# Optimization experiments

Measured on AMD Instinct MI355X. Metric: run time of the kernel, lower is better.

The kernel has to match this reference:

```python
import jax, jax.numpy as jnp
import numpy as np
import math

D_MODEL = 1024
NHEAD = 16
FACTOR = 1
B, L = 2, 4096


def setup_inputs() -> dict:
    key = jax.random.key(0)
    ks = jax.random.split(key, 12)
    s = 0.02
    inp = {
        "query": jax.random.normal(ks[0], (B, L, D_MODEL), dtype=jnp.float32),
        "key": jax.random.normal(ks[1], (B, L, D_MODEL), dtype=jnp.float32),
        "value": jax.random.normal(ks[2], (B, L, D_MODEL), dtype=jnp.float32),
        "Wq": jax.random.normal(ks[3], (D_MODEL, D_MODEL), dtype=jnp.float32) * s,
        "bq": jnp.zeros((D_MODEL,), dtype=jnp.float32),
        "Wk": jax.random.normal(ks[4], (D_MODEL, D_MODEL), dtype=jnp.float32) * s,
        "bk": jnp.zeros((D_MODEL,), dtype=jnp.float32),
        "Wv": jax.random.normal(ks[5], (D_MODEL, D_MODEL), dtype=jnp.float32) * s,
        "bv": jnp.zeros((D_MODEL,), dtype=jnp.float32),
        "Wo": jax.random.normal(ks[6], (D_MODEL, D_MODEL), dtype=jnp.float32) * s,
        "bo": jnp.zeros((D_MODEL,), dtype=jnp.float32),
    }
    return inp


def _autocorr_forward(query, key, value, Wq, bq, Wk, bk, Wv, bv, Wo, bo):
    Bq, Lq, d = query.shape
    Lk = key.shape[1]
    H = NHEAD
    Dk = d // H

    # projections, split heads -> (B, H, L, Dk)
    Q = (query @ Wq + bq).reshape(Bq, Lq, H, Dk).transpose(0, 2, 1, 3)
    K = (key @ Wk + bk).reshape(Bq, Lk, H, Dk).transpose(0, 2, 1, 3)
    V = (value @ Wv + bv).reshape(Bq, Lk, H, Dk).transpose(0, 2, 1, 3)

    # align K/V sequence length to L_q (truncate or zero-pad)
    if Lk > Lq:
        K = K[:, :, :Lq, :]
        V = V[:, :, :Lq, :]
    elif Lq > Lk:
        pad = [(0, 0), (0, 0), (0, Lq - Lk), (0, 0)]
        K = jnp.pad(K, pad)
        V = jnp.pad(V, pad)
    Lloc = Lq

    # FFT-based circular autocorrelation along the sequence axis
    Qf = jnp.fft.rfft(Q, axis=2)
    Kf = jnp.fft.rfft(K, axis=2)
    corr = jnp.fft.irfft(Qf * jnp.conj(Kf), n=Lloc, axis=2)  # (B,H,L,Dk)
    corr_mean = corr.mean(axis=-1)  # (B,H,L)

    top_k = min(max(1, int(FACTOR * math.log(Lloc + 1))), Lloc)
    w, idx = jax.lax.top_k(corr_mean, top_k)  # (B,H,k)
    w = jax.nn.softmax(w, axis=-1)

    # circular gather of V at each delay, weighted combine over top-k delays
    ar = jnp.arange(Lloc)
    shifted = (ar[None, None, None, :] + idx[..., None]) % Lloc  # (B,H,k,L)
    rolled = jnp.take_along_axis(
        V[:, :, None, :, :], shifted[..., None], axis=3
    )  # (B,H,k,L,Dk)
    out = jnp.einsum("bhk,bhkld->bhld", w, rolled)  # (B,H,L,Dk)

    out = out.transpose(0, 2, 1, 3).reshape(Bq, Lq, d)
    return out @ Wo + bo  # dropout is identity in eval mode


def reference(query, key, value, Wq, bq, Wk, bk, Wv, bv, Wo, bo):
    return _autocorr_forward(query, key, value, Wq, bq, Wk, bk, Wv, bv, Wo, bo)
```

## Files before the change

### kernel.cpp

```cpp
#include <hip/hip_runtime.h>
#include <hip/hip_bf16.h>

#define LL 4096
#define NH 16
#define DM 1024
#define DK 64
#define MTOT 8192
#define PI_F 3.14159265358979323846f

typedef short short8 __attribute__((ext_vector_type(8)));
typedef float f32x4 __attribute__((ext_vector_type(4)));

typedef __attribute__((address_space(1))) const unsigned char g_u8;
typedef __attribute__((address_space(3))) unsigned char l_u8;

__device__ __forceinline__ void gload16(const void* g, void* l){
  __builtin_amdgcn_global_load_lds((g_u8*)g, (l_u8*)l, 16, 0, 0);
}

__device__ __forceinline__ unsigned short f2bf(float x){
  union { float f; unsigned int u; } v; v.f = x;
  unsigned int r = v.u + 0x7FFFu + ((v.u >> 16) & 1u);
  return (unsigned short)(r >> 16);
}
__device__ __forceinline__ float bf2f(unsigned short u){
  union { unsigned int u; float f; } v; v.u = ((unsigned int)u) << 16; return v.f;
}

__global__ void k_conv_x(const float* __restrict__ in, unsigned short* __restrict__ out, int n4){
  int i = blockIdx.x*256 + threadIdx.x;
  if (i >= n4) return;
  float4 v = ((const float4*)in)[i];
  ushort4 o; o.x=f2bf(v.x); o.y=f2bf(v.y); o.z=f2bf(v.z); o.w=f2bf(v.w);
  ((ushort4*)out)[i] = o;
}

__global__ void k_conv_x_split2(const float* __restrict__ q, const float* __restrict__ k,
                                unsigned short* __restrict__ hi, unsigned short* __restrict__ lo, int n4){
  int i = blockIdx.x*256 + threadIdx.x;
  float4 v = (i < n4) ? ((const float4*)q)[i] : ((const float4*)k)[i - n4];
  ushort4 oh, ol;
  oh.x=f2bf(v.x); ol.x=f2bf(v.x - bf2f(oh.x));
  oh.y=f2bf(v.y); ol.y=f2bf(v.y - bf2f(oh.y));
  oh.z=f2bf(v.z); ol.z=f2bf(v.z - bf2f(oh.z));
  oh.w=f2bf(v.w); ol.w=f2bf(v.w - bf2f(oh.w));
  ((ushort4*)hi)[i] = oh;
  ((ushort4*)lo)[i] = ol;
}

__global__ void k_conv_wt(const float* __restrict__ W0, const float* __restrict__ W1,
                          const float* __restrict__ W2, const float* __restrict__ W3,
                          unsigned short* __restrict__ hi_base, unsigned short* __restrict__ lo_base){
  const float* W = (blockIdx.z==0)?W0:(blockIdx.z==1)?W1:(blockIdx.z==2)?W2:W3;
  unsigned short* oh = hi_base + (size_t)blockIdx.z*DM*DM;
  unsigned short* ol = (blockIdx.z<2) ? (lo_base + (size_t)blockIdx.z*DM*DM) : nullptr;
  __shared__ unsigned short th[64][65];
  __shared__ unsigned short tl[64][65];
  int n0 = blockIdx.x*64, k0 = blockIdx.y*64;
  for (int i=0;i<16;i++){
    int g = i*256 + threadIdx.x;
    int kr = g>>6, nc = g&63;
    float x = W[(size_t)(k0+kr)*DM + n0+nc];
    unsigned short h = f2bf(x);
    th[kr][nc] = h;
    tl[kr][nc] = f2bf(x - bf2f(h));
  }
  __syncthreads();
  for (int i=0;i<16;i++){
    int g = i*256 + threadIdx.x;
    int nr = g>>6, kc = g&63;
    oh[(size_t)(n0+nr)*DM + k0+kc] = th[kc][nr];
    if (ol) ol[(size_t)(n0+nr)*DM + k0+kc] = tl[kc][nr];
  }
}

template<int MODE>
__global__ __launch_bounds__(256) void k_gemm_plain(
    const short* __restrict__ A, const short* __restrict__ Bt,
    const float* __restrict__ bias, float* __restrict__ Cf, unsigned short* __restrict__ Cb)
{
  __shared__ short As[128][64];
  __shared__ short Bs[128][64];
  const int m0 = blockIdx.x*128, n0 = blockIdx.y*128;
  const int tid = threadIdx.x;
  const int wave = tid>>6, lane = tid&63;
  const int wm = (wave>>1)*64, wn = (wave&1)*64;
  const int li = lane&15, lk4 = lane>>4;
  const int srow = lane>>3;
  const int scol = (((lane&7) ^ srow))*8;
  f32x4 acc[4][4] = {};
  for (int kt=0; kt<16; ++kt){
    #pragma unroll
    for (int c=0;c<4;c++){
      int q = wave*4+c;
      int row = q*8 + srow;
      gload16(&A [(size_t)(m0+row)*DM + kt*64 + scol], &As[q*8][0]);
      gload16(&Bt[(size_t)(n0+row)*DM + kt*64 + scol], &Bs[q*8][0]);
    }
    __syncthreads();
    #pragma unroll
    for (int kk=0; kk<64; kk+=32){
      short8 af[4], bfv[4];
      #pragma unroll
      for (int mi=0;mi<4;mi++)
        af[mi] = *(const short8*)&As[wm+mi*16+li][((( (kk>>3)+lk4 ) ^ (li&7)))*8];
      #pragma unroll
      for (int ni=0;ni<4;ni++)
        bfv[ni] = *(const short8*)&Bs[wn+ni*16+li][((( (kk>>3)+lk4 ) ^ (li&7)))*8];
      #pragma unroll
      for (int mi=0;mi<4;mi++)
        #pragma unroll
        for (int ni=0;ni<4;ni++)
          acc[mi][ni] = __builtin_amdgcn_mfma_f32_16x16x32_bf16(af[mi], bfv[ni], acc[mi][ni], 0,0,0);
    }
    __syncthreads();
  }
  #pragma unroll
  for (int mi=0;mi<4;mi++){
    #pragma unroll
    for (int ni=0;ni<4;ni++){
      const int col = n0 + wn + ni*16 + li;
      const float bv = bias[col];
      const int mbase = m0 + wm + mi*16 + lk4*4;
      #pragma unroll
      for (int r=0;r<4;r++){
        const int row = mbase + r;
        float v = acc[mi][ni][r] + bv;
        if (MODE==2){
          Cf[(size_t)row*DM + col] = v;
        } else {
          int b = row>>12, l = row&(LL-1), h = col>>6, d = col&63;
          Cb[(((size_t)(b*NH+h))*LL + l)*DK + d] = f2bf(v);
        }
      }
    }
  }
}

__global__ __launch_bounds__(512, 2) void k_gemm_split256(
    const short* __restrict__ Ahi, const short* __restrict__ Alo,
    const short* __restrict__ Whi, const short* __restrict__ Wlo,
    const float* __restrict__ bias_q, const float* __restrict__ bias_k,
    float* __restrict__ OutQ, float* __restrict__ OutK, int nq)
{
  __shared__ short AsH[2][256][32];
  __shared__ short AsL[2][256][32];
  __shared__ short BsH[2][256][32];
  __shared__ short BsL[2][256][32];

  const int side = (blockIdx.x >= nq) ? 1 : 0;
  const int m0 = blockIdx.x*256, n0 = blockIdx.y*256;
  const short* Bhi = Whi + (size_t)side*DM*DM;
  const short* Blo = Wlo + (size_t)side*DM*DM;
  const float* bias = side ? bias_k : bias_q;
  float* Ct = side ? OutK : OutQ;
  const int ml0 = m0 - side*(nq*256);

  const int tid = threadIdx.x;
  const int wave = tid>>6, lane = tid&63;
  const int wm = (wave>>2)*128;
  const int wn = (wave&3)*64;
  const int li = lane&15, lk4 = lane>>4;

  const int sr = lane>>2, sc4 = lane&3;
  const int scol = ((sc4 ^ (sr&3) ^ ((sr>>2)&3)))*8;
  const int rbyte = ((lk4 ^ (li&3) ^ (li>>2)))*8;

  f32x4 acc[8][4] = {};

  auto STAGE_HALF = [&](int kt, int bufi, int h){
    const int r0 = h*128 + wave*16;
    const int gr = r0 + sr;
    const int kof = kt*32 + scol;
    gload16(&Ahi[(size_t)(m0+gr)*DM + kof], &AsH[bufi][r0][0]);
    gload16(&Alo[(size_t)(m0+gr)*DM + kof], &AsL[bufi][r0][0]);
    gload16(&Bhi[(size_t)(n0+gr)*DM + kof], &BsH[bufi][r0][0]);
    gload16(&Blo[(size_t)(n0+gr)*DM + kof], &BsL[bufi][r0][0]);
  };

  STAGE_HALF(0, 0, 0);
  STAGE_HALF(0, 0, 1);

  for (int kt=0; kt<32; ++kt){
    const int cur = kt&1;
    if (kt < 31){
      STAGE_HALF(kt+1, cur^1, 0);
      asm volatile("s_waitcnt vmcnt(4)" ::: "memory");
    } else {
      asm volatile("s_waitcnt vmcnt(0)" ::: "memory");
    }
    asm volatile("" ::: "memory");
    __builtin_amdgcn_s_barrier();
    asm volatile("" ::: "memory");

    short8 bhf[4], blf[4];
    #pragma unroll
    for (int ni=0;ni<4;ni++){
      bhf[ni] = *(const short8*)&BsH[cur][wn+ni*16+li][rbyte];
      blf[ni] = *(const short8*)&BsL[cur][wn+ni*16+li][rbyte];
    }
    #pragma unroll
    for (int p=0;p<4;p++){
      if (p==2 && kt<31) STAGE_HALF(kt+1, cur^1, 1);
      short8 ah0 = *(const short8*)&AsH[cur][wm+(2*p  )*16+li][rbyte];
      short8 al0 = *(const short8*)&AsL[cur][wm+(2*p  )*16+li][rbyte];
      short8 ah1 = *(const short8*)&AsH[cur][wm+(2*p+1)*16+li][rbyte];
      short8 al1 = *(const short8*)&AsL[cur][wm+(2*p+1)*16+li][rbyte];
      __builtin_amdgcn_s_setprio(1);
      #pragma unroll
      for (int ni=0;ni<4;ni++){
        f32x4 a0 = acc[2*p][ni];
        a0 = __builtin_amdgcn_mfma_f32_16x16x32_bf16(ah0, bhf[ni], a0, 0,0,0);
        a0 = __builtin_amdgcn_mfma_f32_16x16x32_bf16(ah0, blf[ni], a0, 0,0,0);
        a0 = __builtin_amdgcn_mfma_f32_16x16x32_bf16(al0, bhf[ni], a0, 0,0,0);
        acc[2*p][ni] = a0;
        f32x4 a1 = acc[2*p+1][ni];
        a1 = __builtin_amdgcn_mfma_f32_16x16x32_bf16(ah1, bhf[ni], a1, 0,0,0);
        a1 = __builtin_amdgcn_mfma_f32_16x16x32_bf16(ah1, blf[ni], a1, 0,0,0);
        a1 = __builtin_amdgcn_mfma_f32_16x16x32_bf16(al1, bhf[ni], a1, 0,0,0);
        acc[2*p+1][ni] = a1;
      }
      __builtin_amdgcn_s_setprio(0);
    }
    asm volatile("" ::: "memory");
    __builtin_amdgcn_s_barrier();
    asm volatile("" ::: "memory");
  }

  #pragma unroll
  for (int mi=0;mi<8;mi++){
    #pragma unroll
    for (int ni=0;ni<4;ni++){
      const int col = n0 + wn + ni*16 + li;
      const float bv = bias[col];
      const int mbase = ml0 + wm + mi*16 + lk4*4;
      const int b = mbase>>12, l0 = mbase&(LL-1);
      const int h = col>>6, d = col&63;
      float4 o;
      o.x = acc[mi][ni][0]+bv; o.y = acc[mi][ni][1]+bv;
      o.z = acc[mi][ni][2]+bv; o.w = acc[mi][ni][3]+bv;
      *(float4*)&Ct[(((size_t)(b*NH+h))*DK + d)*LL + l0] = o;
    }
  }
}

__device__ __forceinline__ float2 cmul(float2 a, float2 b){
  return make_float2(a.x*b.x - a.y*b.y, a.x*b.y + a.y*b.x);
}
__device__ __forceinline__ int swz(int i){ return i ^ ((i>>4)&15); }

__device__ __forceinline__ float2 ctw(float2 v, int k, float sgn){
  float c, s;
  switch(k){
    case 0: return v;
    case 1: c= 0.92387953251f; s= 0.38268343236f; break;
    case 2: c= 0.70710678119f; s= 0.70710678119f; break;
    case 3: c= 0.38268343236f; s= 0.92387953251f; break;
    case 4: c= 0.f;            s= 1.f;            break;
    case 6: c=-0.70710678119f; s= 0.70710678119f; break;
    default:c=-0.92387953251f; s=-0.38268343236f; break;
  }
  s *= sgn;
  return make_float2(v.x*c - v.y*s, v.x*s + v.y*c);
}

template<int SGN>
__device__ __forceinline__ void dft16(float2 x[16]){
  const float sg = (float)SGN;
  #pragma unroll
  for (int m1=0;m1<4;m1++){
    float2 a=x[m1], b=x[m1+4], c=x[m1+8], d=x[m1+12];
    float acx=a.x+c.x, acy=a.y+c.y, sx=a.x-c.x, sy=a.y-c.y;
    float bdx=b.x+d.x, bdy=b.y+d.y, tx=b.x-d.x, ty=b.y-d.y;
    float ix=-sg*ty, iy=sg*tx;
    x[m1]    = make_float2(acx+bdx, acy+bdy);
    x[m1+4]  = make_float2(sx+ix,  sy+iy);
    x[m1+8]  = make_float2(acx-bdx, acy-bdy);
    x[m1+12] = make_float2(sx-ix,  sy-iy);
  }
  float2 y[16];
  #pragma unroll
  for (int p1=0;p1<4;p1++){
    float2 a = x[4*p1+0];
    float2 b = ctw(x[4*p1+1], p1,   sg);
    float2 c = ctw(x[4*p1+2], 2*p1, sg);
    float2 d = ctw(x[4*p1+3], 3*p1, sg);
    float acx=a.x+c.x, acy=a.y+c.y, sx=a.x-c.x, sy=a.y-c.y;
    float bdx=b.x+d.x, bdy=b.y+d.y, tx=b.x-d.x, ty=b.y-d.y;
    float ix=-sg*ty, iy=sg*tx;
    y[p1]    = make_float2(acx+bdx, acy+bdy);
    y[p1+4]  = make_float2(sx+ix,  sy+iy);
    y[p1+8]  = make_float2(acx-bdx, acy-bdy);
    y[p1+12] = make_float2(sx-ix,  sy-iy);
  }
  #pragma unroll
  for (int i=0;i<16;i++) x[i]=y[i];
}

template<int SGN>
__device__ __forceinline__ void twiddle_apply(float2 x[16], int j, float invden){
  float th = (float)SGN * 6.28318530717958647f * (float)j * invden;
  float s, c; __sincosf(th, &s, &c);
  float2 w1 = make_float2(c, s);
  float2 w2 = cmul(w1,w1), w3 = cmul(w2,w1), w4 = cmul(w2,w2);
  float2 w8 = cmul(w4,w4), w12 = cmul(w8,w4);
  float2 wl[4] = {make_float2(1.f,0.f), w1, w2, w3};
  float2 wh[4] = {make_float2(1.f,0.f), w4, w8, w12};
  #pragma unroll
  for (int m=1;m<16;m++){
    float2 tw = cmul(wh[m>>2], wl[m&3]);
    x[m] = cmul(x[m], tw);
  }
}

template<int SGN>
__device__ __forceinline__ void fft_stages(float2* lds, float2 x[16], int t){
  dft16<SGN>(x);
  #pragma unroll
  for (int p=0;p<16;p++) lds[swz(t*16+p)] = x[p];
  __syncthreads();
  #pragma unroll
  for (int m=0;m<16;m++) x[m] = lds[swz(t + 256*m)];
  __syncthreads();
  twiddle_apply<SGN>(x, t&15, 1.0f/256.0f);
  dft16<SGN>(x);
  {
    int base = (t>>4)*256 + (t&15);
    #pragma unroll
    for (int p=0;p<16;p++) lds[swz(base + 16*p)] = x[p];
  }
  __syncthreads();
  #pragma unroll
  for (int m=0;m<16;m++) x[m] = lds[swz(t + 256*m)];
  __syncthreads();
  twiddle_apply<SGN>(x, t, 1.0f/4096.0f);
  dft16<SGN>(x);
  #pragma unroll
  for (int p=0;p<16;p++) lds[swz(t + 256*p)] = x[p];
  __syncthreads();
}

__global__ __launch_bounds__(256) void k_fft_fwd(const float* __restrict__ Qt, const float* __restrict__ Kt,
                                                 float* __restrict__ Spart){
  __shared__ float2 lds[4096];
  const int bh = blockIdx.x >> 4, g = blockIdx.x & 15;
  const int t = threadIdx.x;
  float2 pacc[16];
  #pragma unroll
  for (int i=0;i<16;i++) pacc[i]=make_float2(0.f,0.f);
  for (int dd=0; dd<4; ++dd){
    const size_t base = ((size_t)bh*DK + g*4 + dd)*LL;
    float2 x[16];
    #pragma unroll
    for (int m=0;m<16;m++){
      int n = t + 256*m;
      x[m] = make_float2(Qt[base+n], Kt[base+n]);
    }
    fft_stages<-1>(lds, x, t);
    #pragma unroll
    for (int i=0;i<16;i++){
      int f = t + 256*i;
      float2 A = lds[swz(f)];
      float2 Bv = lds[swz((LL-f)&(LL-1))];
      float qr = 0.5f*(A.x+Bv.x), qi = 0.5f*(A.y-Bv.y);
      float kr = 0.5f*(A.y+Bv.y), ki = -0.5f*(A.x-Bv.x);
      pacc[i].x += qr*kr + qi*ki;
      pacc[i].y += qi*kr - qr*ki;
    }
    __syncthreads();
  }
  float2* Sp = (float2*)Spart + (size_t)blockIdx.x*LL;
  #pragma unroll
  for (int i=0;i<16;i++) Sp[t + 256*i] = pacc[i];
}

__global__ __launch_bounds__(256) void k_ifft_topk(const float* __restrict__ Spart,
                                                   float* __restrict__ w8, int* __restrict__ idx8){
  __shared__ float2 lds[4096];
  __shared__ float c[4096];
  __shared__ float rv[256];
  __shared__ int   ri[256];
  __shared__ float topv[8];
  __shared__ int   topi[8];
  const int bh = blockIdx.x, t = threadIdx.x;
  float2 x[16];
  #pragma unroll
  for (int m=0;m<16;m++){
    float2 acc = make_float2(0.f,0.f);
    int n = t + 256*m;
    for (int g2=0; g2<16; ++g2){
      float2 v = ((const float2*)Spart)[((size_t)bh*16+g2)*LL + n];
      acc.x += v.x; acc.y += v.y;
    }
    x[m] = acc;
  }
  fft_stages<1>(lds, x, t);
  const float scale = 1.0f/((float)LL * (float)DK);
  #pragma unroll
  for (int m=0;m<16;m++){ int f=t+256*m; c[f] = lds[swz(f)].x * scale; }
  __syncthreads();
  for (int kk=0; kk<8; kk++){
    float bv = -3.4e38f; int bi = 0;
    #pragma unroll
    for (int i=0;i<16;i++){
      int f = t + 256*i;
      float v = c[f];
      if (v > bv || (v == bv && f < bi)) { bv = v; bi = f; }
    }
    rv[t]=bv; ri[t]=bi;
    __syncthreads();
    for (int off=128; off>0; off>>=1){
      if (t < off){
        float ov = rv[t+off]; int oi = ri[t+off];
        if (ov > rv[t] || (ov == rv[t] && oi < ri[t])) { rv[t]=ov; ri[t]=oi; }
      }
      __syncthreads();
    }
    if (t==0){ topv[kk]=rv[0]; topi[kk]=ri[0]; c[ri[0]] = -3.0e38f; }
    __syncthreads();
  }
  if (t==0){
    float m = topv[0];
    float e[8], sum=0.f;
    for (int k=0;k<8;k++){ e[k]=__expf(topv[k]-m); sum+=e[k]; }
    for (int k=0;k<8;k++){ w8[bh*8+k]=e[k]/sum; idx8[bh*8+k]=topi[k]; }
  }
}

__global__ __launch_bounds__(256) void k_gather(const unsigned short* __restrict__ Vh,
                                                const float* __restrict__ w8, const int* __restrict__ idx8,
                                                unsigned short* __restrict__ Ob){
  const int blk = blockIdx.x;
  const int bh = blk >> 6;
  const int l0 = (blk & 63) * 64;
  const int b = bh >> 4, h = bh & 15;
  float w[8]; int ix[8];
  #pragma unroll
  for (int k=0;k<8;k++){ w[k]=w8[bh*8+k]; ix[k]=idx8[bh*8+k]; }
  const int tid = threadIdx.x;
  for (int it=0; it<16; ++it){
    int e = it*256 + tid;
    int lo = e >> 6, d = e & 63;
    int l = l0 + lo;
    float acc = 0.f;
    #pragma unroll
    for (int k=0;k<8;k++){
      int sl = (l + ix[k]) & (LL-1);
      acc += w[k] * bf2f(Vh[((size_t)bh*LL + sl)*DK + d]);
    }
    Ob[((size_t)(b*LL + l))*DM + h*DK + d] = f2bf(acc);
  }
}

extern "C" void kernel_launch(void* const* d_in, const int* in_sizes, int n_in,
                              void* d_out, int out_size, void* d_ws, size_t ws_size,
                              hipStream_t stream) {
  const float* query = (const float*)d_in[0];
  const float* key   = (const float*)d_in[1];
  const float* value = (const float*)d_in[2];
  const float* Wq = (const float*)d_in[3];
  const float* bq = (const float*)d_in[4];
  const float* Wk = (const float*)d_in[5];
  const float* bk = (const float*)d_in[6];
  const float* Wv = (const float*)d_in[7];
  const float* bv = (const float*)d_in[8];
  const float* Wo = (const float*)d_in[9];
  const float* bo = (const float*)d_in[10];
  float* out = (float*)d_out;

  char* ws = (char*)d_ws;
  const int n4 = MTOT*DM/4;
  const size_t MB16 = (size_t)MTOT*DM*2;

  size_t off = 0;
  auto take = [&](size_t b)->char*{ char* p = ws + off; off += (b + 255) & ~(size_t)255; return p; };

  const size_t merged_bytes = 2*(2*MB16) + (size_t)4*DM*DM*2 + (size_t)2*DM*DM*2
                            + 2*((size_t)2*NH*DK*LL*4) + 16384;

  if (ws_size >= merged_bytes) {
    short* Xs_hi = (short*)take(2*MB16);
    short* Xs_lo = (short*)take(2*MB16);
    short* Wth = (short*)take((size_t)4*DM*DM*2);
    short* Wtl = (short*)take((size_t)2*DM*DM*2);
    float* Qt  = (float*)take((size_t)2*NH*DK*LL*4);
    float* Kt  = (float*)take((size_t)2*NH*DK*LL*4);
    float* w8  = (float*)take(32*8*4);
    int*  idx8 = (int*)take(32*8*4);
    float* Spart = (float*)Xs_hi;
    unsigned short* Ob = (unsigned short*)((char*)Xs_hi + MB16);
    unsigned short* Xv = (unsigned short*)Xs_lo;
    unsigned short* Vh = (unsigned short*)((char*)Xs_lo + MB16);

    k_conv_wt<<<dim3(16,16,4),256,0,stream>>>(Wq,Wk,Wv,Wo,(unsigned short*)Wth,(unsigned short*)Wtl);
    k_conv_x_split2<<<2*n4/256,256,0,stream>>>(query,key,(unsigned short*)Xs_hi,(unsigned short*)Xs_lo,n4);
    k_gemm_split256<<<dim3(64,4),512,0,stream>>>(Xs_hi, Xs_lo, Wth, Wtl, bq, bk, Qt, Kt, 32);
    k_conv_x<<<n4/256,256,0,stream>>>(value, Xv, n4);
    k_gemm_plain<1><<<dim3(64,8),256,0,stream>>>((const short*)Xv, Wth + (size_t)2*DM*DM, bv, nullptr, Vh);
    k_fft_fwd<<<512,256,0,stream>>>(Qt, Kt, Spart);
    k_ifft_topk<<<32,256,0,stream>>>(Spart, w8, idx8);
    k_gather<<<2048,256,0,stream>>>(Vh, w8, idx8, Ob);
    k_gemm_plain<2><<<dim3(64,8),256,0,stream>>>((const short*)Ob, Wth + (size_t)3*DM*DM, bo, out, nullptr);
  } else {
    short* Xhi = (short*)take(MB16);
    short* Xlo = (short*)take(MB16);
    short* Wth = (short*)take((size_t)4*DM*DM*2);
    short* Wtl = (short*)take((size_t)2*DM*DM*2);
    float* Qt  = (float*)take((size_t)2*NH*DK*LL*4);
    float* Kt  = (float*)take((size_t)2*NH*DK*LL*4);
    unsigned short* Vh = (unsigned short*)take((size_t)2*NH*LL*DK*2);
    float* w8  = (float*)take(32*8*4);
    int*  idx8 = (int*)take(32*8*4);
    float* Spart = (float*)Xlo;

    k_conv_wt<<<dim3(16,16,4),256,0,stream>>>(Wq,Wk,Wv,Wo,(unsigned short*)Wth,(unsigned short*)Wtl);

    k_conv_x_split2<<<n4/256,256,0,stream>>>(query,query,(unsigned short*)Xhi,(unsigned short*)Xlo,n4);
    k_gemm_split256<<<dim3(32,4),512,0,stream>>>(Xhi, Xlo, Wth, Wtl, bq, bq, Qt, Qt, 32);

    k_conv_x_split2<<<n4/256,256,0,stream>>>(key,key,(unsigned short*)Xhi,(unsigned short*)Xlo,n4);
    k_gemm_split256<<<dim3(32,4),512,0,stream>>>(Xhi, Xlo, Wth + (size_t)DM*DM, Wtl + (size_t)DM*DM,
                                                 bk, bk, Kt, Kt, 32);

    k_conv_x<<<n4/256,256,0,stream>>>(value,(unsigned short*)Xhi,n4);
    k_gemm_plain<1><<<dim3(64,8),256,0,stream>>>(Xhi, Wth + (size_t)2*DM*DM, bv, nullptr, Vh);

    k_fft_fwd<<<512,256,0,stream>>>(Qt, Kt, Spart);
    k_ifft_topk<<<32,256,0,stream>>>(Spart, w8, idx8);
    k_gather<<<2048,256,0,stream>>>(Vh, w8, idx8, (unsigned short*)Xhi);

    k_gemm_plain<2><<<dim3(64,8),256,0,stream>>>(Xhi, Wth + (size_t)3*DM*DM, bo, out, nullptr);
  }
}
```

Measured before the change: 250.8 us.

## Fuse V projection GEMM into merged Q/K split-precision GEMM launch

Extends the merged Q/K split-bf16 GEMM kernel with a third block range that computes the V projection in single bf16 and writes head-major bf16 output. A new workspace tier lays out separate buffers so the V input conversion and all three projections run in one 96x4 grid, removing the separate k_gemm_plain<1> launch. The intent is to cut launch overhead and fill the GPU better with more blocks. The risk is that V blocks use a 256-tile, 512-thread config with scalar strided stores, and the extra register and LDS pressure from the new branch could affect the Q/K path.

```diff
diff --git a/kernel.cpp b/kernel.cpp
--- a/kernel.cpp
+++ b/kernel.cpp
@@ -139,22 +139,22 @@
 
 __global__ __launch_bounds__(512, 2) void k_gemm_split256(
     const short* __restrict__ Ahi, const short* __restrict__ Alo,
+    const short* __restrict__ Av,
     const short* __restrict__ Whi, const short* __restrict__ Wlo,
+    const short* __restrict__ Wvh,
     const float* __restrict__ bias_q, const float* __restrict__ bias_k,
-    float* __restrict__ OutQ, float* __restrict__ OutK, int nq)
+    const float* __restrict__ bias_v,
+    float* __restrict__ OutQ, float* __restrict__ OutK,
+    unsigned short* __restrict__ OutV, int nq)
 {
   __shared__ short AsH[2][256][32];
   __shared__ short AsL[2][256][32];
   __shared__ short BsH[2][256][32];
   __shared__ short BsL[2][256][32];
 
-  const int side = (blockIdx.x >= nq) ? 1 : 0;
-  const int m0 = blockIdx.x*256, n0 = blockIdx.y*256;
-  const short* Bhi = Whi + (size_t)side*DM*DM;
-  const short* Blo = Wlo + (size_t)side*DM*DM;
-  const float* bias = side ? bias_k : bias_q;
-  float* Ct = side ? OutK : OutQ;
-  const int ml0 = m0 - side*(nq*256);
+  const int bx = blockIdx.x;
+  const int side = (bx >= 2*nq) ? 2 : (bx >= nq) ? 1 : 0;
+  const int n0 = blockIdx.y*256;
 
   const int tid = threadIdx.x;
   const int wave = tid>>6, lane = tid&63;
@@ -168,78 +168,152 @@
 
   f32x4 acc[8][4] = {};
 
-  auto STAGE_HALF = [&](int kt, int bufi, int h){
-    const int r0 = h*128 + wave*16;
-    const int gr = r0 + sr;
-    const int kof = kt*32 + scol;
-    gload16(&Ahi[(size_t)(m0+gr)*DM + kof], &AsH[bufi][r0][0]);
-    gload16(&Alo[(size_t)(m0+gr)*DM + kof], &AsL[bufi][r0][0]);
-    gload16(&Bhi[(size_t)(n0+gr)*DM + kof], &BsH[bufi][r0][0]);
-    gload16(&Blo[(size_t)(n0+gr)*DM + kof], &BsL[bufi][r0][0]);
-  };
-
-  STAGE_HALF(0, 0, 0);
-  STAGE_HALF(0, 0, 1);
-
-  for (int kt=0; kt<32; ++kt){
-    const int cur = kt&1;
-    if (kt < 31){
-      STAGE_HALF(kt+1, cur^1, 0);
-      asm volatile("s_waitcnt vmcnt(4)" ::: "memory");
-    } else {
-      asm volatile("s_waitcnt vmcnt(0)" ::: "memory");
-    }
-    asm volatile("" ::: "memory");
-    __builtin_amdgcn_s_barrier();
-    asm volatile("" ::: "memory");
-
-    short8 bhf[4], blf[4];
-    #pragma unroll
-    for (int ni=0;ni<4;ni++){
-      bhf[ni] = *(const short8*)&BsH[cur][wn+ni*16+li][rbyte];
-      blf[ni] = *(const short8*)&BsL[cur][wn+ni*16+li][rbyte];
-    }
-    #pragma unroll
-    for (int p=0;p<4;p++){
-      if (p==2 && kt<31) STAGE_HALF(kt+1, cur^1, 1);
-      short8 ah0 = *(const short8*)&AsH[cur][wm+(2*p  )*16+li][rbyte];
-      short8 al0 = *(const short8*)&AsL[cur][wm+(2*p  )*16+li][rbyte];
-      short8 ah1 = *(const short8*)&AsH[cur][wm+(2*p+1)*16+li][rbyte];
-      short8 al1 = *(const short8*)&AsL[cur][wm+(2*p+1)*16+li][rbyte];
-      __builtin_amdgcn_s_setprio(1);
+  if (side < 2){
+    const int m0 = bx*256;
+    const short* Bhi = Whi + (size_t)side*DM*DM;
+    const short* Blo = Wlo + (size_t)side*DM*DM;
+    const float* bias = side ? bias_k : bias_q;
+    float* Ct = side ? OutK : OutQ;
+    const int ml0 = m0 - side*(nq*256);
+
+    auto STAGE_HALF = [&](int kt, int bufi, int h){
+      const int r0 = h*128 + wave*16;
+      const int gr = r0 + sr;
+      const int kof = kt*32 + scol;
+      gload16(&Ahi[(size_t)(m0+gr)*DM + kof], &AsH[bufi][r0][0]);
+      gload16(&Alo[(size_t)(m0+gr)*DM + kof], &AsL[bufi][r0][0]);
+      gload16(&Bhi[(size_t)(n0+gr)*DM + kof], &BsH[bufi][r0][0]);
+      gload16(&Blo[(size_t)(n0+gr)*DM + kof], &BsL[bufi][r0][0]);
+    };
+
+    STAGE_HALF(0, 0, 0);
+    STAGE_HALF(0, 0, 1);
+
+    for (int kt=0; kt<32; ++kt){
+      const int cur = kt&1;
+      if (kt < 31){
+        STAGE_HALF(kt+1, cur^1, 0);
+        asm volatile("s_waitcnt vmcnt(4)" ::: "memory");
+      } else {
+        asm volatile("s_waitcnt vmcnt(0)" ::: "memory");
+      }
+      asm volatile("" ::: "memory");
+      __builtin_amdgcn_s_barrier();
+      asm volatile("" ::: "memory");
+
+      short8 bhf[4], blf[4];
       #pragma unroll
       for (int ni=0;ni<4;ni++){
-        f32x4 a0 = acc[2*p][ni];
-        a0 = __builtin_amdgcn_mfma_f32_16x16x32_bf16(ah0, bhf[ni], a0, 0,0,0);
-        a0 = __builtin_amdgcn_mfma_f32_16x16x32_bf16(ah0, blf[ni], a0, 0,0,0);
-        a0 = __builtin_amdgcn_mfma_f32_16x16x32_bf16(al0, bhf[ni], a0, 0,0,0);
-        acc[2*p][ni] = a0;
-        f32x4 a1 = acc[2*p+1][ni];
-        a1 = __builtin_amdgcn_mfma_f32_16x16x32_bf16(ah1, bhf[ni], a1, 0,0,0);
-        a1 = __builtin_amdgcn_mfma_f32_16x16x32_bf16(ah1, blf[ni], a1, 0,0,0);
-        a1 = __builtin_amdgcn_mfma_f32_16x16x32_bf16(al1, bhf[ni], a1, 0,0,0);
-        acc[2*p+1][ni] = a1;
-      }
-      __builtin_amdgcn_s_setprio(0);
-    }
-    asm volatile("" ::: "memory");
-    __builtin_amdgcn_s_barrier();
-    asm volatile("" ::: "memory");
-  }
-
-  #pragma unroll
-  for (int mi=0;mi<8;mi++){
-    #pragma unroll
-    for (int ni=0;ni<4;ni++){
-      const int col = n0 + wn + ni*16 + li;
-      const float bv = bias[col];
-      const int mbase = ml0 + wm + mi*16 + lk4*4;
-      const int b = mbase>>12, l0 = mbase&(LL-1);
-      const int h = col>>6, d = col&63;
-      float4 o;
-      o.x = acc[mi][ni][0]+bv; o.y = acc[mi][ni][1]+bv;
-      o.z = acc[mi][ni][2]+bv; o.w = acc[mi][ni][3]+bv;
-      *(float4*)&Ct[(((size_t)(b*NH+h))*DK + d)*LL + l0] = o;
+        bhf[ni] = *(const short8*)&BsH[cur][wn+ni*16+li][rbyte];
+        blf[ni] = *(const short8*)&BsL[cur][wn+ni*16+li][rbyte];
+      }
+      #pragma unroll
+      for (int p=0;p<4;p++){
+        if (p==2 && kt<31) STAGE_HALF(kt+1, cur^1, 1);
+        short8 ah0 = *(const short8*)&AsH[cur][wm+(2*p  )*16+li][rbyte];
+        short8 al0 = *(const short8*)&AsL[cur][wm+(2*p  )*16+li][rbyte];
+        short8 ah1 = *(const short8*)&AsH[cur][wm+(2*p+1)*16+li][rbyte];
+        short8 al1 = *(const short8*)&AsL[cur][wm+(2*p+1)*16+li][rbyte];
+        __builtin_amdgcn_s_setprio(1);
+        #pragma unroll
+        for (int ni=0;ni<4;ni++){
+          f32x4 a0 = acc[2*p][ni];
+          a0 = __builtin_amdgcn_mfma_f32_16x16x32_bf16(ah0, bhf[ni], a0, 0,0,0);
+          a0 = __builtin_amdgcn_mfma_f32_16x16x32_bf16(ah0, blf[ni], a0, 0,0,0);
+          a0 = __builtin_amdgcn_mfma_f32_16x16x32_bf16(al0, bhf[ni], a0, 0,0,0);
+          acc[2*p][ni] = a0;
+          f32x4 a1 = acc[2*p+1][ni];
+          a1 = __builtin_amdgcn_mfma_f32_16x16x32_bf16(ah1, bhf[ni], a1, 0,0,0);
+          a1 = __builtin_amdgcn_mfma_f32_16x16x32_bf16(ah1, blf[ni], a1, 0,0,0);
+          a1 = __builtin_amdgcn_mfma_f32_16x16x32_bf16(al1, bhf[ni], a1, 0,0,0);
+          acc[2*p+1][ni] = a1;
+        }
+        __builtin_amdgcn_s_setprio(0);
+      }
+      asm volatile("" ::: "memory");
+      __builtin_amdgcn_s_barrier();
+      asm volatile("" ::: "memory");
+    }
+
+    #pragma unroll
+    for (int mi=0;mi<8;mi++){
+      #pragma unroll
+      for (int ni=0;ni<4;ni++){
+        const int col = n0 + wn + ni*16 + li;
+        const float bv = bias[col];
+        const int mbase = ml0 + wm + mi*16 + lk4*4;
+        const int b = mbase>>12, l0 = mbase&(LL-1);
+        const int h = col>>6, d = col&63;
+        float4 o;
+        o.x = acc[mi][ni][0]+bv; o.y = acc[mi][ni][1]+bv;
+        o.z = acc[mi][ni][2]+bv; o.w = acc[mi][ni][3]+bv;
+        *(float4*)&Ct[(((size_t)(b*NH+h))*DK + d)*LL + l0] = o;
+      }
+    }
+  } else {
+    const int m0 = (bx - 2*nq)*256;
+
+    auto STAGE_HALF_V = [&](int kt, int bufi, int h){
+      const int r0 = h*128 + wave*16;
+      const int gr = r0 + sr;
+      const int kof = kt*32 + scol;
+      gload16(&Av [(size_t)(m0+gr)*DM + kof], &AsH[bufi][r0][0]);
+      gload16(&Wvh[(size_t)(n0+gr)*DM + kof], &BsH[bufi][r0][0]);
+    };
+
+    STAGE_HALF_V(0, 0, 0);
+    STAGE_HALF_V(0, 0, 1);
+
+    for (int kt=0; kt<32; ++kt){
+      const int cur = kt&1;
+      if (kt < 31){
+        STAGE_HALF_V(kt+1, cur^1, 0);
+        asm volatile("s_waitcnt vmcnt(2)" ::: "memory");
+      } else {
+        asm volatile("s_waitcnt vmcnt(0)" ::: "memory");
+      }
+      asm volatile("" ::: "memory");
+      __builtin_amdgcn_s_barrier();
+      asm volatile("" ::: "memory");
+
+      short8 bhf[4];
+      #pragma unroll
+      for (int ni=0;ni<4;ni++)
+        bhf[ni] = *(const short8*)&BsH[cur][wn+ni*16+li][rbyte];
+
+      #pragma unroll
+      for (int p=0;p<4;p++){
+        if (p==2 && kt<31) STAGE_HALF_V(kt+1, cur^1, 1);
+        short8 ah0 = *(const short8*)&AsH[cur][wm+(2*p  )*16+li][rbyte];
+        short8 ah1 = *(const short8*)&AsH[cur][wm+(2*p+1)*16+li][rbyte];
+        __builtin_amdgcn_s_setprio(1);
+        #pragma unroll
+        for (int ni=0;ni<4;ni++){
+          acc[2*p][ni]   = __builtin_amdgcn_mfma_f32_16x16x32_bf16(ah0, bhf[ni], acc[2*p][ni],   0,0,0);
+          acc[2*p+1][ni] = __builtin_amdgcn_mfma_f32_16x16x32_bf16(ah1, bhf[ni], acc[2*p+1][ni], 0,0,0);
+        }
+        __builtin_amdgcn_s_setprio(0);
+      }
+      asm volatile("" ::: "memory");
+      __builtin_amdgcn_s_barrier();
+      asm volatile("" ::: "memory");
+    }
+
+    #pragma unroll
+    for (int mi=0;mi<8;mi++){
+      #pragma unroll
+      for (int ni=0;ni<4;ni++){
+        const int col = n0 + wn + ni*16 + li;
+        const float bv = bias_v[col];
+        const int mbase = m0 + wm + mi*16 + lk4*4;
+        const int h = col>>6, d = col&63;
+        #pragma unroll
+        for (int r=0;r<4;r++){
+          const int row = mbase + r;
+          const int b = row>>12, l = row&(LL-1);
+          OutV[(((size_t)(b*NH+h))*LL + l)*DK + d] = f2bf(acc[mi][ni][r] + bv);
+        }
+      }
     }
   }
 }
@@ -475,10 +549,35 @@
   size_t off = 0;
   auto take = [&](size_t b)->char*{ char* p = ws + off; off += (b + 255) & ~(size_t)255; return p; };
 
-  const size_t merged_bytes = 2*(2*MB16) + (size_t)4*DM*DM*2 + (size_t)2*DM*DM*2
-                            + 2*((size_t)2*NH*DK*LL*4) + 16384;
-
-  if (ws_size >= merged_bytes) {
+  const size_t tier2_bytes = 2*(2*MB16) + (size_t)4*DM*DM*2 + (size_t)2*DM*DM*2
+                           + 2*((size_t)2*NH*DK*LL*4) + 16384;
+  const size_t tier1_bytes = tier2_bytes + 2*MB16;
+
+  if (ws_size >= tier1_bytes) {
+    short* Xs_hi = (short*)take(2*MB16);
+    short* Xs_lo = (short*)take(2*MB16);
+    unsigned short* Xv = (unsigned short*)take(MB16);
+    unsigned short* Vh = (unsigned short*)take(MB16);
+    short* Wth = (short*)take((size_t)4*DM*DM*2);
+    short* Wtl = (short*)take((size_t)2*DM*DM*2);
+    float* Qt  = (float*)take((size_t)2*NH*DK*LL*4);
+    float* Kt  = (float*)take((size_t)2*NH*DK*LL*4);
+    float* w8  = (float*)take(32*8*4);
+    int*  idx8 = (int*)take(32*8*4);
+    float* Spart = (float*)Xs_hi;
+    unsigned short* Ob = (unsigned short*)((char*)Xs_hi + MB16);
+
+    k_conv_wt<<<dim3(16,16,4),256,0,stream>>>(Wq,Wk,Wv,Wo,(unsigned short*)Wth,(unsigned short*)Wtl);
+    k_conv_x_split2<<<2*n4/256,256,0,stream>>>(query,key,(unsigned short*)Xs_hi,(unsigned short*)Xs_lo,n4);
+    k_conv_x<<<n4/256,256,0,stream>>>(value, Xv, n4);
+    k_gemm_split256<<<dim3(96,4),512,0,stream>>>(Xs_hi, Xs_lo, (const short*)Xv,
+                                                 Wth, Wtl, Wth + (size_t)2*DM*DM,
+                                                 bq, bk, bv, Qt, Kt, Vh, 32);
+    k_fft_fwd<<<512,256,0,stream>>>(Qt, Kt, Spart);
+    k_ifft_topk<<<32,256,0,stream>>>(Spart, w8, idx8);
+    k_gather<<<2048,256,0,stream>>>(Vh, w8, idx8, Ob);
+    k_gemm_plain<2><<<dim3(64,8),256,0,stream>>>((const short*)Ob, Wth + (size_t)3*DM*DM, bo, out, nullptr);
+  } else if (ws_size >= tier2_bytes) {
     short* Xs_hi = (short*)take(2*MB16);
     short* Xs_lo = (short*)take(2*MB16);
     short* Wth = (short*)take((size_t)4*DM*DM*2);
@@ -494,7 +593,9 @@
 
     k_conv_wt<<<dim3(16,16,4),256,0,stream>>>(Wq,Wk,Wv,Wo,(unsigned short*)Wth,(unsigned short*)Wtl);
     k_conv_x_split2<<<2*n4/256,256,0,stream>>>(query,key,(unsigned short*)Xs_hi,(unsigned short*)Xs_lo,n4);
-    k_gemm_split256<<<dim3(64,4),512,0,stream>>>(Xs_hi, Xs_lo, Wth, Wtl, bq, bk, Qt, Kt, 32);
+    k_gemm_split256<<<dim3(64,4),512,0,stream>>>(Xs_hi, Xs_lo, Xs_hi,
+                                                 Wth, Wtl, Wth,
+                                                 bq, bk, bv, Qt, Kt, (unsigned short*)Qt, 32);
     k_conv_x<<<n4/256,256,0,stream>>>(value, Xv, n4);
     k_gemm_plain<1><<<dim3(64,8),256,0,stream>>>((const short*)Xv, Wth + (size_t)2*DM*DM, bv, nullptr, Vh);
     k_fft_fwd<<<512,256,0,stream>>>(Qt, Kt, Spart);
@@ -516,11 +617,13 @@
     k_conv_wt<<<dim3(16,16,4),256,0,stream>>>(Wq,Wk,Wv,Wo,(unsigned short*)Wth,(unsigned short*)Wtl);
 
     k_conv_x_split2<<<n4/256,256,0,stream>>>(query,query,(unsigned short*)Xhi,(unsigned short*)Xlo,n4);
-    k_gemm_split256<<<dim3(32,4),512,0,stream>>>(Xhi, Xlo, Wth, Wtl, bq, bq, Qt, Qt, 32);
+    k_gemm_split256<<<dim3(32,4),512,0,stream>>>(Xhi, Xlo, Xhi, Wth, Wtl, Wth,
+                                                 bq, bq, bq, Qt, Qt, (unsigned short*)Qt, 32);
 
     k_conv_x_split2<<<n4/256,256,0,stream>>>(key,key,(unsigned short*)Xhi,(unsigned short*)Xlo,n4);
-    k_gemm_split256<<<dim3(32,4),512,0,stream>>>(Xhi, Xlo, Wth + (size_t)DM*DM, Wtl + (size_t)DM*DM,
-                                                 bk, bk, Kt, Kt, 32);
+    k_gemm_split256<<<dim3(32,4),512,0,stream>>>(Xhi, Xlo, Xhi,
+                                                 Wth + (size_t)DM*DM, Wtl + (size_t)DM*DM, Wth,
+                                                 bk, bk, bk, Kt, Kt, (unsigned short*)Kt, 32);
 
     k_conv_x<<<n4/256,256,0,stream>>>(value,(unsigned short*)Xhi,n4);
     k_gemm_plain<1><<<dim3(64,8),256,0,stream>>>(Xhi, Wth + (size_t)2*DM*DM, bv, nullptr, Vh);
```

After: 308.0 us. 1.23x slower.
